# Kernel tuning notes

Measured on AMD Instinct MI355X. Metric: run time of the kernel, lower is better.

## Reference

```python
import jax, jax.numpy as jnp
import numpy as np

N_HEADS = 12


def _sink_window_visible(S, num_sink_tokens, window_size):
    # visible[i, j] = (j <= i) and (j < num_sink or j >= i - window + 1)
    i = jnp.arange(S)[:, None]
    j = jnp.arange(S)[None, :]
    return (j <= i) & ((j < num_sink_tokens) | (j >= i - window_size + 1))


def setup_inputs() -> dict:
    key = jax.random.key(0)
    k1, k2, k3 = jax.random.split(key, 3)
    B, S, D = 1, 4096, 768
    hidden_states = jax.random.normal(k1, (B, S, D), dtype=jnp.float32)
    w_attn = jax.random.normal(k2, (D, 3 * D), dtype=jnp.float32) * 0.02
    b_attn = jnp.zeros((3 * D,), dtype=jnp.float32)
    w_proj = jax.random.normal(k3, (D, D), dtype=jnp.float32) * 0.02
    b_proj = jnp.zeros((D,), dtype=jnp.float32)
    return {
        "hidden_states": hidden_states,
        "w_attn": w_attn,
        "b_attn": b_attn,
        "w_proj": w_proj,
        "b_proj": b_proj,
        "num_sink_tokens": 4,
        "window_size": 256,
    }


def reference(hidden_states, w_attn, b_attn, w_proj, b_proj, num_sink_tokens, window_size):
    B, S, D = hidden_states.shape
    H = N_HEADS
    hd = D // H
    # GPT-2 fused qkv projection (Conv1D): x @ W + b
    qkv = hidden_states @ w_attn + b_attn  # [B, S, 3D]
    q, k, v = jnp.split(qkv, 3, axis=-1)
    q = q.reshape(B, S, H, hd).transpose(0, 2, 1, 3)  # [B, H, S, hd]
    k = k.reshape(B, S, H, hd).transpose(0, 2, 1, 3)
    v = v.reshape(B, S, H, hd).transpose(0, 2, 1, 3)
    scale = 1.0 / jnp.sqrt(jnp.asarray(hd, dtype=q.dtype))
    scores = jnp.einsum("bhqd,bhkd->bhqk", q, k) * scale  # [B, H, S, S]
    visible = _sink_window_visible(S, num_sink_tokens, window_size)  # [S, S]
    neg = jnp.finfo(scores.dtype).min
    scores = jnp.where(visible[None, None, :, :], scores, neg)
    attn = jax.nn.softmax(scores, axis=-1)
    ctx = jnp.einsum("bhqk,bhkd->bhqd", attn, v)  # [B, H, S, hd]
    ctx = ctx.transpose(0, 2, 1, 3).reshape(B, S, D)
    return ctx @ w_proj + b_proj
```

## Files before the change

kernel.cpp:

```cpp
#include <hip/hip_runtime.h>
#include <hip/hip_bf16.h>
#include <stdint.h>

typedef short bf16x8 __attribute__((ext_vector_type(8)));
typedef unsigned short u16x8 __attribute__((ext_vector_type(8)));
typedef float f32x4 __attribute__((ext_vector_type(4)));

__device__ inline unsigned short f2bf(float f) {
    union { float f; uint32_t u; } v; v.f = f;
    uint32_t lsb = (v.u >> 16) & 1u;
    v.u += 0x7fffu + lsb;
    return (unsigned short)(v.u >> 16);
}

__device__ inline uint32_t cvt_pk_bf16(float lo, float hi) {
    uint32_t r;
    asm("v_cvt_pk_bf16_f32 %0, %1, %2" : "=v"(r) : "v"(lo), "v"(hi));
    return r;
}

__device__ inline void gload16(const unsigned short* g, unsigned short* l) {
    __builtin_amdgcn_global_load_lds(
        (const __attribute__((address_space(1))) unsigned int*)g,
        (__attribute__((address_space(3))) unsigned int*)l, 16, 0, 0);
}

__global__ __launch_bounds__(256) void prep(const float* __restrict__ x,
                                            const float* __restrict__ wa,
                                            const float* __restrict__ wp,
                                            unsigned short* __restrict__ xbf,
                                            unsigned short* __restrict__ waT,
                                            unsigned short* __restrict__ wpT) {
    __shared__ float tile[64][65];
    const int t = threadIdx.x;
    const int id = blockIdx.x;
    if (id < 1536) {
        const int i = id * 256 + t;
        const float4* p = (const float4*)x + (size_t)i * 2;
        float4 a = p[0], b = p[1];
        u16x8 o;
        o[0] = f2bf(a.x); o[1] = f2bf(a.y); o[2] = f2bf(a.z); o[3] = f2bf(a.w);
        o[4] = f2bf(b.x); o[5] = f2bf(b.y); o[6] = f2bf(b.z); o[7] = f2bf(b.w);
        *((u16x8*)xbf + i) = o;
        return;
    }
    const float* in; unsigned short* out; int R, C, bx, by;
    if (id < 1968) { int k = id - 1536; in = wa; out = waT; R = 768; C = 2304; bx = k % 36; by = k / 36; }
    else           { int k = id - 1968; in = wp; out = wpT; R = 768; C = 768;  bx = k % 12; by = k / 12; }
    const int r0 = by * 64, c0 = bx * 64;
    {
        int r = t >> 2, cs = t & 3;
        #pragma unroll
        for (int i = 0; i < 4; ++i) {
            int c = (cs * 4 + i) * 4;
            float4 v = *(const float4*)(in + (size_t)(r0 + r) * C + c0 + c);
            tile[r][c] = v.x; tile[r][c + 1] = v.y; tile[r][c + 2] = v.z; tile[r][c + 3] = v.w;
        }
    }
    __syncthreads();
    {
        int c = t >> 2, rs = t & 3;
        #pragma unroll
        for (int i = 0; i < 2; ++i) {
            u16x8 o;
            #pragma unroll
            for (int e = 0; e < 8; ++e) o[e] = f2bf(tile[rs * 16 + i * 8 + e][c]);
            *(u16x8*)(out + (size_t)(c0 + c) * R + r0 + rs * 16 + i * 8) = o;
        }
    }
}

template <int OUT_BF16, int WRITE_VT>
__global__ __launch_bounds__(256) void gemm_bf16(const unsigned short* __restrict__ A,
                                                 const unsigned short* __restrict__ BT,
                                                 const float* __restrict__ bias,
                                                 void* __restrict__ Cout,
                                                 unsigned short* __restrict__ vTout,
                                                 int M, int N, int K) {
    __shared__ unsigned short As[2][128 * 64];
    __shared__ unsigned short Bs[2][128 * 64];
    const int tid = threadIdx.x;
    const int lane = tid & 63;
    const int w = tid >> 6;
    const int wr = w >> 1, wc = w & 1;
    const int row0 = blockIdx.y * 128, col0 = blockIdx.x * 128;

    const int srow = lane >> 3;
    const int sseg = (lane & 7) ^ srow;

    const int nt = K >> 6;

    f32x4 acc[4][4] = {};

#define STAGE(buf, k0)                                                                     \
    {                                                                                      \
        _Pragma("unroll")                                                                  \
        for (int i = 0; i < 4; ++i) {                                                      \
            const int ch = w * 4 + i;                                                      \
            const int r = ch * 8 + srow;                                                   \
            gload16(A + (size_t)(row0 + r) * K + (k0) + sseg * 8, &As[buf][ch * 512]);     \
            gload16(BT + (size_t)(col0 + r) * K + (k0) + sseg * 8, &Bs[buf][ch * 512]);    \
        }                                                                                  \
    }

    STAGE(0, 0);
    int cur = 0;
    for (int t = 0; t < nt; ++t) {
        __syncthreads();
        if (t + 1 < nt) {
            if (cur) STAGE(0, (t + 1) << 6) else STAGE(1, (t + 1) << 6);
        }
        const unsigned short* as = As[cur];
        const unsigned short* bs = Bs[cur];
        const int c0s = ((0 + (lane >> 4)) ^ (lane & 7)) << 3;
        const int c1s = ((4 + (lane >> 4)) ^ (lane & 7)) << 3;
        bf16x8 af[2][4], bfr[2][4];
        #pragma unroll
        for (int m = 0; m < 4; ++m) {
            const int ra = (wr * 64 + m * 16 + (lane & 15)) * 64;
            const int rb = (wc * 64 + m * 16 + (lane & 15)) * 64;
            af[0][m]  = *(const bf16x8*)(as + ra + c0s);
            af[1][m]  = *(const bf16x8*)(as + ra + c1s);
            bfr[0][m] = *(const bf16x8*)(bs + rb + c0s);
            bfr[1][m] = *(const bf16x8*)(bs + rb + c1s);
        }
        #pragma unroll
        for (int ks = 0; ks < 2; ++ks)
            #pragma unroll
            for (int m = 0; m < 4; ++m)
                #pragma unroll
                for (int n = 0; n < 4; ++n)
                    acc[m][n] = __builtin_amdgcn_mfma_f32_16x16x32_bf16(af[ks][m], bfr[ks][n], acc[m][n], 0, 0, 0);
        cur ^= 1;
    }
#undef STAGE

    if (WRITE_VT && col0 >= 1536) {
        #pragma unroll
        for (int m = 0; m < 4; ++m) {
            int row = row0 + wr * 64 + m * 16 + (lane >> 4) * 4;
            #pragma unroll
            for (int n = 0; n < 4; ++n) {
                int col = col0 + wc * 64 + n * 16 + (lane & 15);
                float bb = bias[col];
                uint2 st;
                st.x = cvt_pk_bf16(acc[m][n][0] + bb, acc[m][n][1] + bb);
                st.y = cvt_pk_bf16(acc[m][n][2] + bb, acc[m][n][3] + bb);
                *(uint2*)(vTout + (size_t)(col - 1536) * 4096 + row) = st;
            }
        }
        return;
    }

    #pragma unroll
    for (int m = 0; m < 4; ++m) {
        int row = row0 + wr * 64 + m * 16 + (lane >> 4) * 4;
        #pragma unroll
        for (int n = 0; n < 4; ++n) {
            int col = col0 + wc * 64 + n * 16 + (lane & 15);
            float bb = bias[col];
            #pragma unroll
            for (int r = 0; r < 4; ++r) {
                float v = acc[m][n][r] + bb;
                if (OUT_BF16)
                    ((unsigned short*)Cout)[(size_t)(row + r) * N + col] = f2bf(v);
                else
                    ((float*)Cout)[(size_t)(row + r) * N + col] = v;
            }
        }
    }
}

__global__ __launch_bounds__(256) void attn_mfma(const unsigned short* __restrict__ qkv,
                                                 const unsigned short* __restrict__ vT,
                                                 unsigned short* __restrict__ ctx,
                                                 const int* __restrict__ pnsink,
                                                 const int* __restrict__ pwin) {
    __shared__ unsigned short Ks[2][64 * 64];
    __shared__ unsigned short Vs[2][64 * 64];
    const int tid = threadIdx.x, lane = tid & 63, w = tid >> 6;
    const int q = lane & 15, g = lane >> 4;
    const int h = blockIdx.y;
    const int bx = ((blockIdx.x & 7) << 3) | (blockIdx.x >> 3);
    const int i0 = bx << 6;
    const int nsink = *pnsink, wsize = *pwin;
    const int D3 = 2304;
    const int iq = i0 + 16 * w + q;

    const int sseg = (lane & 7) ^ (lane >> 3);

    const unsigned short* qrow = qkv + (size_t)iq * D3 + h * 64 + g * 8;
    const bf16x8 aq0 = *(const bf16x8*)(qrow);
    const bf16x8 aq1 = *(const bf16x8*)(qrow + 32);

    float m_run = -1e30f, l_run = 0.f;
    f32x4 octx[4] = {};

    int wlo = i0 - wsize + 1; if (wlo < 0) wlo = 0;
    const int t_lo = (wlo >> 6) << 6;
    const int ntiles = ((i0 - t_lo) >> 6) + 1 + (t_lo > 0 ? 1 : 0);

    const int sl01 = q + ((g & 1) << 5);
    const int sl23 = sl01 + 16;
    const int x7 = q & 7;
    const int ck0 = ((0 + g) ^ x7) << 3;
    const int ck1 = ((4 + g) ^ x7) << 3;

#define ASTAGE(buf, kb)                                                                \
    {                                                                                  \
        _Pragma("unroll")                                                              \
        for (int i = 0; i < 2; ++i) {                                                  \
            const int ch = w * 2 + i;                                                  \
            const int r = ch * 8 + (lane >> 3);                                        \
            gload16(qkv + (size_t)((kb) + r) * D3 + 768 + h * 64 + sseg * 8,           \
                    &Ks[buf][ch * 512]);                                               \
            gload16(vT + ((size_t)h * 64 + r) * 4096 + (kb) + sseg * 8,                \
                    &Vs[buf][ch * 512]);                                               \
        }                                                                              \
    }

    auto kb_of = [&](int tt, bool& so) -> int {
        if (t_lo > 0) { so = (tt == 0); return so ? 0 : t_lo + ((tt - 1) << 6); }
        so = false; return tt << 6;
    };

    { bool s0; ASTAGE(0, kb_of(0, s0)); }
    int cur = 0;
    for (int tt = 0; tt < ntiles; ++tt) {
        __syncthreads();
        if (tt + 1 < ntiles) {
            bool sx; int kbn = kb_of(tt + 1, sx);
            if (cur) ASTAGE(0, kbn) else ASTAGE(1, kbn);
        }
        bool sink_only; const int kb = kb_of(tt, sink_only);
        const int nbmax = (sink_only && nsink <= 16) ? 1 : 4;
        const int ksmax = (nbmax == 1) ? 1 : 2;
        const unsigned short* ks_ = Ks[cur];
        const unsigned short* vs_ = Vs[cur];

        f32x4 sacc[4] = {};
        #pragma unroll
        for (int nb = 0; nb < 4; ++nb) {
            if (nb < nbmax) {
                const int rr = (nb * 16 + q) * 64;
                bf16x8 k0 = *(const bf16x8*)(ks_ + rr + ck0);
                bf16x8 k1 = *(const bf16x8*)(ks_ + rr + ck1);
                sacc[nb] = __builtin_amdgcn_mfma_f32_16x16x32_bf16(k0, aq0, sacc[nb], 0, 0, 0);
                sacc[nb] = __builtin_amdgcn_mfma_f32_16x16x32_bf16(k1, aq1, sacc[nb], 0, 0, 0);
            }
        }
        float vmax = -1e30f;
        #pragma unroll
        for (int nb = 0; nb < 4; ++nb)
            #pragma unroll
            for (int r = 0; r < 4; ++r) {
                int j = kb + nb * 16 + g * 4 + r;
                bool vis = (j <= iq) && ((j < nsink) || (j > iq - wsize));
                sacc[nb][r] = vis ? sacc[nb][r] * 0.125f : -1e30f;
                vmax = fmaxf(vmax, sacc[nb][r]);
            }
        vmax = fmaxf(vmax, __shfl_xor(vmax, 16));
        vmax = fmaxf(vmax, __shfl_xor(vmax, 32));
        const float mn = fmaxf(m_run, vmax);
        const float alpha = __expf(m_run - mn);
        const bool dead = (mn <= -1e29f);
        float p[4][4];
        float lsum = 0.f;
        #pragma unroll
        for (int nb = 0; nb < 4; ++nb)
            #pragma unroll
            for (int r = 0; r < 4; ++r) {
                float pv = dead ? 0.f : __expf(sacc[nb][r] - mn);
                p[nb][r] = pv;
                lsum += pv;
            }
        lsum += __shfl_xor(lsum, 16);
        lsum += __shfl_xor(lsum, 32);
        l_run = l_run * alpha + lsum;
        m_run = mn;
        #pragma unroll
        for (int nb = 0; nb < 4; ++nb)
            #pragma unroll
            for (int r = 0; r < 4; ++r) octx[nb][r] *= alpha;

        uint32_t c01[4][2];
        #pragma unroll
        for (int nb = 0; nb < 4; ++nb) {
            c01[nb][0] = cvt_pk_bf16(p[nb][0], p[nb][1]);
            c01[nb][1] = cvt_pk_bf16(p[nb][2], p[nb][3]);
        }
        #pragma unroll
        for (int ks = 0; ks < 2; ++ks) {
            if (ks < ksmax) {
                uint32_t f00 = (uint32_t)__shfl((int)c01[2 * ks + 0][0], sl01);
                uint32_t f01 = (uint32_t)__shfl((int)c01[2 * ks + 1][0], sl01);
                uint32_t f10 = (uint32_t)__shfl((int)c01[2 * ks + 0][1], sl01);
                uint32_t f11 = (uint32_t)__shfl((int)c01[2 * ks + 1][1], sl01);
                uint32_t f20 = (uint32_t)__shfl((int)c01[2 * ks + 0][0], sl23);
                uint32_t f21 = (uint32_t)__shfl((int)c01[2 * ks + 1][0], sl23);
                uint32_t f30 = (uint32_t)__shfl((int)c01[2 * ks + 0][1], sl23);
                uint32_t f31 = (uint32_t)__shfl((int)c01[2 * ks + 1][1], sl23);
                union { uint32_t u[4]; bf16x8 v; } pa;
                pa.u[0] = (g >> 1) ? f01 : f00;
                pa.u[1] = (g >> 1) ? f11 : f10;
                pa.u[2] = (g >> 1) ? f21 : f20;
                pa.u[3] = (g >> 1) ? f31 : f30;
                const int cv = ((ks * 4 + g) ^ x7) << 3;
                #pragma unroll
                for (int nb = 0; nb < 4; ++nb) {
                    bf16x8 bv = *(const bf16x8*)(vs_ + (nb * 16 + q) * 64 + cv);
                    octx[nb] = __builtin_amdgcn_mfma_f32_16x16x32_bf16(bv, pa.v, octx[nb], 0, 0, 0);
                }
            }
        }
        cur ^= 1;
    }
#undef ASTAGE

    const float inv = (l_run > 0.f) ? 1.f / l_run : 0.f;
    unsigned short* crow = ctx + (size_t)iq * 768 + h * 64 + g * 4;
    #pragma unroll
    for (int nb = 0; nb < 4; ++nb) {
        uint2 st;
        st.x = cvt_pk_bf16(octx[nb][0] * inv, octx[nb][1] * inv);
        st.y = cvt_pk_bf16(octx[nb][2] * inv, octx[nb][3] * inv);
        *(uint2*)(crow + nb * 16) = st;
    }
}

extern "C" void kernel_launch(void* const* d_in, const int* in_sizes, int n_in,
                              void* d_out, int out_size, void* d_ws, size_t ws_size,
                              hipStream_t stream) {
    const float* x      = (const float*)d_in[0];
    const float* w_attn = (const float*)d_in[1];
    const float* b_attn = (const float*)d_in[2];
    const float* w_proj = (const float*)d_in[3];
    const float* b_proj = (const float*)d_in[4];
    const int*   pnsink = (const int*)d_in[5];
    const int*   pwin   = (const int*)d_in[6];
    float* out = (float*)d_out;

    const int D = 768, S = 4096, N1 = 3 * D;

    unsigned short* xbf   = (unsigned short*)d_ws;
    unsigned short* waT   = xbf + (size_t)S * D;
    unsigned short* wpT   = waT + (size_t)N1 * D;
    unsigned short* qkvbf = wpT + (size_t)D * D;
    unsigned short* ctxbf = qkvbf + (size_t)S * N1;
    unsigned short* vTbf  = ctxbf + (size_t)S * D;

    prep<<<2112, 256, 0, stream>>>(x, w_attn, w_proj, xbf, waT, wpT);

    {
        dim3 g(N1 / 128, S / 128);
        gemm_bf16<1, 1><<<g, 256, 0, stream>>>(xbf, waT, b_attn, qkvbf, vTbf, S, N1, D);
    }
    {
        dim3 g(S / 64, 12);
        attn_mfma<<<g, 256, 0, stream>>>(qkvbf, vTbf, ctxbf, pnsink, pwin);
    }
    {
        dim3 g(D / 128, S / 128);
        gemm_bf16<0, 0><<<g, 256, 0, stream>>>(ctxbf, wpT, b_proj, out, nullptr, S, D, D);
    }
}
```

Before: 72.10 us.

## Fold sink tokens into first window tile and add lazy softmax rescaling

The separate sink-only tile is removed. The first 16 sink keys and values are loaded into extra LDS rows alongside the first window tile, and an extra MFMA block processes them in the same iteration. This cuts one pipeline stage and one barrier per block. The softmax moves to exp2 with log2e folded into the scale, and rescaling of the accumulator is skipped unless the running max grows by more than a threshold. s_setprio hints are added around the MFMA sections. Extra LDS use and the threshold-based lazy rescale carry overflow and precision risk, and sinks beyond 16 tokens are no longer handled.

```diff
diff --git a/kernel.cpp b/kernel.cpp
--- a/kernel.cpp
+++ b/kernel.cpp
@@ -176,8 +176,10 @@
                                                  unsigned short* __restrict__ ctx,
                                                  const int* __restrict__ pnsink,
                                                  const int* __restrict__ pwin) {
-    __shared__ unsigned short Ks[2][64 * 64];
-    __shared__ unsigned short Vs[2][64 * 64];
+    __shared__ unsigned short Ks0[80 * 64];
+    __shared__ unsigned short Vs0[64 * 64 + 2 * 64 * 8];
+    __shared__ unsigned short Ks1[64 * 64];
+    __shared__ unsigned short Vs1[64 * 64];
     const int tid = threadIdx.x, lane = tid & 63, w = tid >> 6;
     const int q = lane & 15, g = lane >> 4;
     const int h = blockIdx.y;
@@ -186,6 +188,7 @@
     const int nsink = *pnsink, wsize = *pwin;
     const int D3 = 2304;
     const int iq = i0 + 16 * w + q;
+    const float SC = 0.18033688011112042f;
 
     const int sseg = (lane & 7) ^ (lane >> 3);
 
@@ -198,7 +201,8 @@
 
     int wlo = i0 - wsize + 1; if (wlo < 0) wlo = 0;
     const int t_lo = (wlo >> 6) << 6;
-    const int ntiles = ((i0 - t_lo) >> 6) + 1 + (t_lo > 0 ? 1 : 0);
+    const bool ext = (t_lo > 0);
+    const int ntiles = ((i0 - t_lo) >> 6) + 1;
 
     const int sl01 = q + ((g & 1) << 5);
     const int sl23 = sl01 + 16;
@@ -206,42 +210,44 @@
     const int ck0 = ((0 + g) ^ x7) << 3;
     const int ck1 = ((4 + g) ^ x7) << 3;
 
-#define ASTAGE(buf, kb)                                                                \
+#define ASTAGE(KSB, VSB, kb)                                                           \
     {                                                                                  \
         _Pragma("unroll")                                                              \
         for (int i = 0; i < 2; ++i) {                                                  \
             const int ch = w * 2 + i;                                                  \
             const int r = ch * 8 + (lane >> 3);                                        \
             gload16(qkv + (size_t)((kb) + r) * D3 + 768 + h * 64 + sseg * 8,           \
-                    &Ks[buf][ch * 512]);                                               \
+                    (KSB) + ch * 512);                                                 \
             gload16(vT + ((size_t)h * 64 + r) * 4096 + (kb) + sseg * 8,                \
-                    &Vs[buf][ch * 512]);                                               \
+                    (VSB) + ch * 512);                                                 \
         }                                                                              \
     }
 
-    auto kb_of = [&](int tt, bool& so) -> int {
-        if (t_lo > 0) { so = (tt == 0); return so ? 0 : t_lo + ((tt - 1) << 6); }
-        so = false; return tt << 6;
-    };
-
-    { bool s0; ASTAGE(0, kb_of(0, s0)); }
-    int cur = 0;
+    ASTAGE(Ks0, Vs0, t_lo);
+    if (ext) {
+        if (w == 0)      gload16(qkv + (size_t)(lane >> 3) * D3 + 768 + h * 64 + sseg * 8, Ks0 + 4096);
+        else if (w == 1) gload16(qkv + (size_t)(8 + (lane >> 3)) * D3 + 768 + h * 64 + sseg * 8, Ks0 + 4096 + 512);
+        else if (w == 2) gload16(vT + ((size_t)h * 64 + lane) * 4096, Vs0 + 4096);
+        else             gload16(vT + ((size_t)h * 64 + lane) * 4096 + 8, Vs0 + 4096 + 1024);
+    }
+
     for (int tt = 0; tt < ntiles; ++tt) {
         __syncthreads();
         if (tt + 1 < ntiles) {
-            bool sx; int kbn = kb_of(tt + 1, sx);
-            if (cur) ASTAGE(0, kbn) else ASTAGE(1, kbn);
-        }
-        bool sink_only; const int kb = kb_of(tt, sink_only);
-        const int nbmax = (sink_only && nsink <= 16) ? 1 : 4;
-        const int ksmax = (nbmax == 1) ? 1 : 2;
-        const unsigned short* ks_ = Ks[cur];
-        const unsigned short* vs_ = Vs[cur];
-
-        f32x4 sacc[4] = {};
-        #pragma unroll
-        for (int nb = 0; nb < 4; ++nb) {
-            if (nb < nbmax) {
+            const int kbn = t_lo + ((tt + 1) << 6);
+            if (tt & 1) ASTAGE(Ks0, Vs0, kbn) else ASTAGE(Ks1, Vs1, kbn);
+        }
+        const int kb = t_lo + (tt << 6);
+        const unsigned short* ks_ = (tt & 1) ? Ks1 : Ks0;
+        const unsigned short* vs_ = (tt & 1) ? Vs1 : Vs0;
+        const bool extt = ext && (tt == 0);
+        const int NB = extt ? 5 : 4;
+
+        f32x4 sacc[5] = {};
+        __builtin_amdgcn_s_setprio(1);
+        #pragma unroll
+        for (int nb = 0; nb < 5; ++nb) {
+            if (nb < NB) {
                 const int rr = (nb * 16 + q) * 64;
                 bf16x8 k0 = *(const bf16x8*)(ks_ + rr + ck0);
                 bf16x8 k1 = *(const bf16x8*)(ks_ + rr + ck1);
@@ -249,71 +255,99 @@
                 sacc[nb] = __builtin_amdgcn_mfma_f32_16x16x32_bf16(k1, aq1, sacc[nb], 0, 0, 0);
             }
         }
+        __builtin_amdgcn_s_setprio(0);
+
         float vmax = -1e30f;
         #pragma unroll
-        for (int nb = 0; nb < 4; ++nb)
-            #pragma unroll
-            for (int r = 0; r < 4; ++r) {
-                int j = kb + nb * 16 + g * 4 + r;
-                bool vis = (j <= iq) && ((j < nsink) || (j > iq - wsize));
-                sacc[nb][r] = vis ? sacc[nb][r] * 0.125f : -1e30f;
-                vmax = fmaxf(vmax, sacc[nb][r]);
-            }
+        for (int nb = 0; nb < 5; ++nb)
+            if (nb < NB)
+                #pragma unroll
+                for (int r = 0; r < 4; ++r) {
+                    const int slot = nb * 16 + g * 4 + r;
+                    const int j = (slot >= 64) ? (slot - 64) : kb + slot;
+                    const bool vis = (j <= iq) && ((j < nsink) || (j > iq - wsize));
+                    sacc[nb][r] = vis ? sacc[nb][r] * SC : -1e30f;
+                    vmax = fmaxf(vmax, sacc[nb][r]);
+                }
         vmax = fmaxf(vmax, __shfl_xor(vmax, 16));
         vmax = fmaxf(vmax, __shfl_xor(vmax, 32));
-        const float mn = fmaxf(m_run, vmax);
-        const float alpha = __expf(m_run - mn);
-        const bool dead = (mn <= -1e29f);
-        float p[4][4];
+
+        const bool upd = !__all(vmax <= m_run + 8.f);
+        if (upd) {
+            const float mn = fmaxf(m_run, vmax);
+            const float alpha = __builtin_amdgcn_exp2f(m_run - mn);
+            l_run *= alpha;
+            #pragma unroll
+            for (int nb = 0; nb < 4; ++nb)
+                #pragma unroll
+                for (int r = 0; r < 4; ++r) octx[nb][r] *= alpha;
+            m_run = mn;
+        }
+        float p[5][4];
         float lsum = 0.f;
         #pragma unroll
-        for (int nb = 0; nb < 4; ++nb)
-            #pragma unroll
-            for (int r = 0; r < 4; ++r) {
-                float pv = dead ? 0.f : __expf(sacc[nb][r] - mn);
-                p[nb][r] = pv;
-                lsum += pv;
-            }
+        for (int nb = 0; nb < 5; ++nb)
+            if (nb < NB)
+                #pragma unroll
+                for (int r = 0; r < 4; ++r) {
+                    const float pv = __builtin_amdgcn_exp2f(sacc[nb][r] - m_run);
+                    p[nb][r] = pv;
+                    lsum += pv;
+                }
         lsum += __shfl_xor(lsum, 16);
         lsum += __shfl_xor(lsum, 32);
-        l_run = l_run * alpha + lsum;
-        m_run = mn;
-        #pragma unroll
-        for (int nb = 0; nb < 4; ++nb)
-            #pragma unroll
-            for (int r = 0; r < 4; ++r) octx[nb][r] *= alpha;
-
-        uint32_t c01[4][2];
-        #pragma unroll
-        for (int nb = 0; nb < 4; ++nb) {
-            c01[nb][0] = cvt_pk_bf16(p[nb][0], p[nb][1]);
-            c01[nb][1] = cvt_pk_bf16(p[nb][2], p[nb][3]);
-        }
+        l_run += lsum;
+
+        uint32_t c01[5][2];
+        #pragma unroll
+        for (int nb = 0; nb < 5; ++nb)
+            if (nb < NB) {
+                c01[nb][0] = cvt_pk_bf16(p[nb][0], p[nb][1]);
+                c01[nb][1] = cvt_pk_bf16(p[nb][2], p[nb][3]);
+            }
+
+        __builtin_amdgcn_s_setprio(1);
         #pragma unroll
         for (int ks = 0; ks < 2; ++ks) {
-            if (ks < ksmax) {
-                uint32_t f00 = (uint32_t)__shfl((int)c01[2 * ks + 0][0], sl01);
-                uint32_t f01 = (uint32_t)__shfl((int)c01[2 * ks + 1][0], sl01);
-                uint32_t f10 = (uint32_t)__shfl((int)c01[2 * ks + 0][1], sl01);
-                uint32_t f11 = (uint32_t)__shfl((int)c01[2 * ks + 1][1], sl01);
-                uint32_t f20 = (uint32_t)__shfl((int)c01[2 * ks + 0][0], sl23);
-                uint32_t f21 = (uint32_t)__shfl((int)c01[2 * ks + 1][0], sl23);
-                uint32_t f30 = (uint32_t)__shfl((int)c01[2 * ks + 0][1], sl23);
-                uint32_t f31 = (uint32_t)__shfl((int)c01[2 * ks + 1][1], sl23);
-                union { uint32_t u[4]; bf16x8 v; } pa;
-                pa.u[0] = (g >> 1) ? f01 : f00;
-                pa.u[1] = (g >> 1) ? f11 : f10;
-                pa.u[2] = (g >> 1) ? f21 : f20;
-                pa.u[3] = (g >> 1) ? f31 : f30;
-                const int cv = ((ks * 4 + g) ^ x7) << 3;
-                #pragma unroll
-                for (int nb = 0; nb < 4; ++nb) {
-                    bf16x8 bv = *(const bf16x8*)(vs_ + (nb * 16 + q) * 64 + cv);
-                    octx[nb] = __builtin_amdgcn_mfma_f32_16x16x32_bf16(bv, pa.v, octx[nb], 0, 0, 0);
-                }
-            }
-        }
-        cur ^= 1;
+            uint32_t f00 = (uint32_t)__shfl((int)c01[2 * ks + 0][0], sl01);
+            uint32_t f01 = (uint32_t)__shfl((int)c01[2 * ks + 1][0], sl01);
+            uint32_t f10 = (uint32_t)__shfl((int)c01[2 * ks + 0][1], sl01);
+            uint32_t f11 = (uint32_t)__shfl((int)c01[2 * ks + 1][1], sl01);
+            uint32_t f20 = (uint32_t)__shfl((int)c01[2 * ks + 0][0], sl23);
+            uint32_t f21 = (uint32_t)__shfl((int)c01[2 * ks + 1][0], sl23);
+            uint32_t f30 = (uint32_t)__shfl((int)c01[2 * ks + 0][1], sl23);
+            uint32_t f31 = (uint32_t)__shfl((int)c01[2 * ks + 1][1], sl23);
+            union { uint32_t u[4]; bf16x8 v; } pa;
+            pa.u[0] = (g >> 1) ? f01 : f00;
+            pa.u[1] = (g >> 1) ? f11 : f10;
+            pa.u[2] = (g >> 1) ? f21 : f20;
+            pa.u[3] = (g >> 1) ? f31 : f30;
+            const int cv = ((ks * 4 + g) ^ x7) << 3;
+            #pragma unroll
+            for (int nb = 0; nb < 4; ++nb) {
+                bf16x8 bv = *(const bf16x8*)(vs_ + (nb * 16 + q) * 64 + cv);
+                octx[nb] = __builtin_amdgcn_mfma_f32_16x16x32_bf16(bv, pa.v, octx[nb], 0, 0, 0);
+            }
+        }
+        if (extt) {
+            uint32_t e0 = (uint32_t)__shfl((int)c01[4][0], sl01);
+            uint32_t e1 = (uint32_t)__shfl((int)c01[4][1], sl01);
+            uint32_t e2 = (uint32_t)__shfl((int)c01[4][0], sl23);
+            uint32_t e3 = (uint32_t)__shfl((int)c01[4][1], sl23);
+            union { uint32_t u[4]; bf16x8 v; } pa;
+            const bool lo = (g < 2);
+            pa.u[0] = lo ? e0 : 0u;
+            pa.u[1] = lo ? e1 : 0u;
+            pa.u[2] = lo ? e2 : 0u;
+            pa.u[3] = lo ? e3 : 0u;
+            const unsigned short* vb = vs_ + 4096 + ((g & 1) << 10);
+            #pragma unroll
+            for (int nb = 0; nb < 4; ++nb) {
+                bf16x8 bv = *(const bf16x8*)(vb + (nb * 16 + q) * 8);
+                octx[nb] = __builtin_amdgcn_mfma_f32_16x16x32_bf16(bv, pa.v, octx[nb], 0, 0, 0);
+            }
+        }
+        __builtin_amdgcn_s_setprio(0);
     }
 #undef ASTAGE
 
```

Measured after the change: 71.07 us. About the same (-1.4%).
